# Kernel tuning notes

Measured on AMD Instinct MI355X. Metric: run time of the kernel, lower is better.

## Reference

```python
import jax, jax.numpy as jnp
import numpy as np

WD, WH, WW = 2, 7, 7          # window size (D,H,W)
NH = 3                        # num heads
DIM = 96                      # channels
N = WD * WH * WW              # tokens per window = 98
HD = DIM // NH                # head dim = 32
MLP_HID = int(DIM * 4.0)
EPS = 1e-5


def _rel_index():
    coords = np.stack(np.meshgrid(np.arange(WD), np.arange(WH), np.arange(WW), indexing='ij')).reshape(3, -1)
    rel = (coords[:, :, None] - coords[:, None, :]).transpose(1, 2, 0)  # (N,N,3)
    rel[:, :, 0] += WD - 1
    rel[:, :, 1] += WH - 1
    rel[:, :, 2] += WW - 1
    rel[:, :, 0] *= (2 * WH - 1) * (2 * WW - 1)
    rel[:, :, 1] *= 2 * WW - 1
    return rel.sum(-1)  # (N,N) int

REL_IDX = jnp.asarray(_rel_index())


def setup_inputs() -> dict:
    key = jax.random.key(0)
    ks = jax.random.split(key, 8)
    s = 0.02
    return {
        'x': jax.random.normal(ks[0], (8, 8, 56, 56, DIM), jnp.float32),
        'norm1_w': jnp.ones((DIM,), jnp.float32),
        'norm1_b': jnp.zeros((DIM,), jnp.float32),
        'qkv_w': jax.random.normal(ks[1], (3 * DIM, DIM), jnp.float32) * s,
        'qkv_b': jnp.zeros((3 * DIM,), jnp.float32),
        'proj_w': jax.random.normal(ks[2], (DIM, DIM), jnp.float32) * s,
        'proj_b': jnp.zeros((DIM,), jnp.float32),
        'rpb_table': jax.random.normal(ks[3], ((2 * WD - 1) * (2 * WH - 1) * (2 * WW - 1), NH), jnp.float32) * s,
        'norm2_w': jnp.ones((DIM,), jnp.float32),
        'norm2_b': jnp.zeros((DIM,), jnp.float32),
        'fc1_w': jax.random.normal(ks[4], (MLP_HID, DIM), jnp.float32) * s,
        'fc1_b': jnp.zeros((MLP_HID,), jnp.float32),
        'fc2_w': jax.random.normal(ks[5], (DIM, MLP_HID), jnp.float32) * s,
        'fc2_b': jnp.zeros((DIM,), jnp.float32),
    }


def _layernorm(x, w, b):
    m = x.mean(-1, keepdims=True)
    v = ((x - m) ** 2).mean(-1, keepdims=True)
    return (x - m) * jax.lax.rsqrt(v + EPS) * w + b


def _window_partition(x):
    B, D, H, W, C = x.shape
    x = x.reshape(B, D // WD, WD, H // WH, WH, W // WW, WW, C)
    return x.transpose(0, 1, 3, 5, 2, 4, 6, 7).reshape(-1, N, C)


def _window_reverse(win, B, D, H, W):
    x = win.reshape(B, D // WD, H // WH, W // WW, WD, WH, WW, -1)
    return x.transpose(0, 1, 4, 2, 5, 3, 6, 7).reshape(B, D, H, W, -1)


def reference(x, norm1_w, norm1_b, qkv_w, qkv_b, proj_w, proj_b, rpb_table,
              norm2_w, norm2_b, fc1_w, fc1_b, fc2_w, fc2_b):
    B, D, H, W, C = x.shape
    shortcut = x
    xn = _layernorm(x, norm1_w, norm1_b)
    xw = _window_partition(xn)                       # (Bw, N, C)
    Bw = xw.shape[0]

    qkv = xw @ qkv_w.T + qkv_b                       # (Bw, N, 3C)
    qkv = qkv.reshape(Bw, N, 3, NH, HD).transpose(2, 0, 3, 1, 4)
    q, k, v = qkv[0], qkv[1], qkv[2]                 # (Bw, NH, N, HD)
    scale = HD ** -0.5
    attn = jnp.einsum('bhnd,bhmd->bhnm', q * scale, k)
    bias = rpb_table[REL_IDX].transpose(2, 0, 1)     # (NH, N, N)
    attn = jax.nn.softmax(attn + bias[None], axis=-1)
    out = jnp.einsum('bhnm,bhmd->bhnd', attn, v)
    out = out.transpose(0, 2, 1, 3).reshape(Bw, N, C)
    out = out @ proj_w.T + proj_b

    x = shortcut + _window_reverse(out, B, D, H, W)
    h = _layernorm(x, norm2_w, norm2_b)
    h = jax.nn.gelu(h @ fc1_w.T + fc1_b, approximate=False)
    x = x + (h @ fc2_w.T + fc2_b)
    return x
```

## Files before the change

### kernel.cpp

```cpp
#include <hip/hip_runtime.h>
#include <hip/hip_bf16.h>
#include <math.h>


#define NTOK 98
#define SCALE 0.17677669529663687f

#define FR_PROJ 54
#define FR_FC1  72
#define FR_FC2  144
#define WS_BF16_N 110592
#define WS_BIASM_BYTE 221184
#define WS_NEED   296448

typedef __attribute__((ext_vector_type(8))) short bf16x8;
typedef __attribute__((ext_vector_type(4))) float f32x4;

__device__ __forceinline__ int row_of(int wid, int t) {
    int b = wid >> 8, rem = wid & 255;
    int d0 = rem >> 6, h0 = (rem >> 3) & 7, w0 = rem & 7;
    int td = t / 49, tr = t % 49, th = tr / 7, tw = tr % 7;
    int dd = d0 * 2 + td, hh = h0 * 7 + th, ww = w0 * 7 + tw;
    return ((b * 8 + dd) * 56 + hh) * 56 + ww;
}

__device__ __forceinline__ int pcode(int t) {
    int a = t / 49, r = t - 49 * a, b = r / 7, c = r - 7 * b;
    return a * 169 + b * 13 + c;
}

__device__ __forceinline__ unsigned short f2bfu(float f) {
    __hip_bfloat16 h = __float2bfloat16(f);
    unsigned short u; __builtin_memcpy(&u, &h, 2); return u;
}
__device__ __forceinline__ unsigned int pk2(float lo, float hi) {
    return (unsigned int)f2bfu(lo) | ((unsigned int)f2bfu(hi) << 16);
}
__device__ __forceinline__ float bl16(unsigned int u) {
    union { unsigned int i; float f; } c; c.i = u << 16; return c.f;
}
__device__ __forceinline__ float bh16(unsigned int u) {
    union { unsigned int i; float f; } c; c.i = u & 0xffff0000u; return c.f;
}
__device__ __forceinline__ bf16x8 loadB_sw(const __hip_bfloat16* wsb, int frag, int lane) {
    return *(const bf16x8*)(wsb + (frag << 9) + (lane << 3));
}
__device__ __forceinline__ bf16x8 ldsFrag(const __hip_bfloat16* base, int frag, int lane) {
    return *(const bf16x8*)(base + (frag << 9) + (lane << 3));
}
__device__ __forceinline__ bf16x8 loadB_f32(const float* wf, int idx) {
    bf16x8 r;
    #pragma unroll
    for (int j = 0; j < 8; ++j) r[j] = (short)f2bfu(wf[idx + j]);
    return r;
}
__device__ __forceinline__ float gelu(float v) {
    return 0.5f * v * (1.f + erff(v * 0.70710678118654752f));
}

__global__ __launch_bounds__(256) void prep_kernel(
    const float* __restrict__ qkv_w, const float* __restrict__ proj_w,
    const float* __restrict__ fc1_w, const float* __restrict__ fc2_w,
    const float* __restrict__ rpb,
    __hip_bfloat16* __restrict__ wsb, __hip_bfloat16* __restrict__ biasMb)
{
    int i = blockIdx.x * 256 + threadIdx.x;
    if (i < WS_BF16_N) {
        int f = i >> 9, lane = (i >> 3) & 63, j = i & 7;
        int l15 = lane & 15, g = lane >> 4;
        float v;
        if (f < FR_PROJ) {
            int ks = f % 3, nt = (f / 3) % 6, c = f / 18;
            v = qkv_w[(c * 96 + nt * 16 + l15) * 96 + ks * 32 + g * 8 + j];
            if (c == 0) v *= SCALE;
        } else if (f < FR_FC1) {
            int f2 = f - FR_PROJ, ks = f2 % 3, nt = f2 / 3;
            v = proj_w[(nt * 16 + l15) * 96 + ks * 32 + g * 8 + j];
        } else if (f < FR_FC2) {
            int f2 = f - FR_FC1, ks = f2 % 3, nt = (f2 / 3) % 4, hc = f2 / 12;
            v = fc1_w[(hc * 64 + nt * 16 + l15) * 96 + ks * 32 + g * 8 + j];
        } else {
            int f2 = f - FR_FC2, p = f2 & 1, nt = (f2 >> 1) % 6, hc = f2 / 12;
            v = fc2_w[(nt * 16 + l15) * 384 + hc * 64 + p * 32 + g * 8 + j];
        }
        wsb[i] = __float2bfloat16(v);
    } else if (i < WS_BF16_N + 37632) {
        int j = i - WS_BF16_N;
        int r = j & 3, lane = (j >> 2) & 63;
        int rest = j >> 8;
        int U = rest % 7; rest /= 7;
        int Tt = rest % 7, h = rest / 7;
        int t = Tt * 16 + (lane & 15);              if (t > 97) t = 97;
        int u = U * 16 + ((lane >> 4) << 2) + r;    if (u > 97) u = 97;
        biasMb[j] = __float2bfloat16(rpb[(pcode(t) - pcode(u) + 253) * 3 + h]);
    }
}

__global__ __launch_bounds__(512, 4) void fused_kernel(
    const float* __restrict__ x,
    const float* __restrict__ n1w, const float* __restrict__ n1b,
    const float* __restrict__ qkv_w, const float* __restrict__ qkv_b,
    const float* __restrict__ proj_w, const float* __restrict__ proj_b,
    const float* __restrict__ rpb,
    const float* __restrict__ n2w, const float* __restrict__ n2b,
    const float* __restrict__ w1, const float* __restrict__ b1,
    const float* __restrict__ w2, const float* __restrict__ b2,
    const __hip_bfloat16* __restrict__ wsb, const __hip_bfloat16* __restrict__ biasMb,
    int usews,
    float* __restrict__ out)
{
    __shared__ __align__(16) unsigned char LB[72704];
    __shared__ int rowbase[NTOK];
    __hip_bfloat16 (*XS)[104] = (__hip_bfloat16 (*)[104])LB;
    __hip_bfloat16 (*Kb)[104] = (__hip_bfloat16 (*)[104])(LB + 23296);
    __hip_bfloat16* VQ = (__hip_bfloat16*)(LB + 46592);
    __hip_bfloat16* S0 = (__hip_bfloat16*)(LB + 23296);
    __hip_bfloat16* S1 = (__hip_bfloat16*)(LB + 47872);

    const int wid = blockIdx.x, tid = threadIdx.x;
    const int lane = tid & 63, wv = tid >> 6;
    const int l15 = lane & 15;
    const int g = lane >> 4;
    const int koff = g * 8;
    const int drow = g * 4;
    const bool oddg = (g >> 1) & 1;
    const int srcA = l15 + ((g & 1) << 5);
    const int srcB = srcA + 16;

    for (int t = tid; t < NTOK; t += 512) rowbase[t] = row_of(wid, t) * 96;
    for (int i = tid; i < 14 * 104; i += 512) {
        int r = 98 + i / 104, c = i % 104;
        XS[r][c] = __float2bfloat16(0.f);
    }
    if (usews) {
        const int4* s = (const int4*)wsb;
        int4* d = (int4*)S0;
        for (int i = tid; i < 1152; i += 512) d[i] = s[i];
    }

    {
        float w0 = n1w[lane], b0 = n1b[lane];
        float w1_ = (lane < 32) ? n1w[64 + lane] : 0.f;
        float b1_ = (lane < 32) ? n1b[64 + lane] : 0.f;
        for (int t = wv; t < NTOK; t += 8) {
            int base = row_of(wid, t) * 96;
            float v0 = x[base + lane];
            float v1 = (lane < 32) ? x[base + 64 + lane] : 0.f;
            float s = v0 + v1;
            #pragma unroll
            for (int m = 32; m; m >>= 1) s += __shfl_xor(s, m, 64);
            float mean = s * (1.f / 96.f);
            float e0 = v0 - mean;
            float e1 = (lane < 32) ? (v1 - mean) : 0.f;
            float ss = e0 * e0 + e1 * e1;
            #pragma unroll
            for (int m = 32; m; m >>= 1) ss += __shfl_xor(ss, m, 64);
            float rstd = rsqrtf(ss * (1.f / 96.f) + 1e-5f);
            XS[t][lane] = __float2bfloat16(e0 * rstd * w0 + b0);
            if (lane < 32)
                XS[t][64 + lane] = __float2bfloat16(e1 * rstd * w1_ + b1_);
        }
    }
    __syncthreads();

    __hip_bfloat16* QB = &VQ[0];
    for (int tile = wv; tile < 42; tile += 8) {
        int m0 = (tile / 6) * 16, nt = tile % 6, n0 = nt * 16;
        f32x4 acc = {0.f, 0.f, 0.f, 0.f};
        #pragma unroll
        for (int ks = 0; ks < 3; ++ks) {
            bf16x8 a = *(const bf16x8*)&XS[m0 + l15][ks * 32 + koff];
            bf16x8 b = usews ? ldsFrag(S0, nt * 3 + ks, lane)
                             : loadB_f32(qkv_w, (n0 + l15) * 96 + ks * 32 + koff);
            acc = __builtin_amdgcn_mfma_f32_16x16x32_bf16(a, b, acc, 0, 0, 0);
        }
        float bb = qkv_b[n0 + l15];
        #pragma unroll
        for (int r = 0; r < 4; ++r) {
            float q = usews ? (acc[r] + bb * SCALE) : ((acc[r] + bb) * SCALE);
            QB[(m0 + drow + r) * 104 + n0 + l15] = __float2bfloat16(q);
        }
    }
    __syncthreads();

    bf16x8 qf[3];
    #pragma unroll
    for (int i = 0; i < 3; ++i) {
        int task = wv + 8 * i;
        if (task < 21) {
            int s_ = task / 3, h_ = task - 3 * s_;
            qf[i] = *(const bf16x8*)&QB[(s_ * 16 + l15) * 104 + h_ * 32 + koff];
        }
    }
    __syncthreads();

    __hip_bfloat16* vT = &VQ[0];
    for (int i = tid; i < 96 * 38; i += 512) {
        int r = i / 38, c = 98 + (i - r * 38);
        vT[r * 136 + c] = __float2bfloat16(0.f);
    }
    for (int c = 1; c < 3; ++c) {
        for (int tile = wv; tile < 42; tile += 8) {
            int m0 = (tile / 6) * 16, nt = tile % 6, n0 = nt * 16;
            f32x4 acc = {0.f, 0.f, 0.f, 0.f};
            #pragma unroll
            for (int ks = 0; ks < 3; ++ks) {
                bf16x8 a = *(const bf16x8*)&XS[m0 + l15][ks * 32 + koff];
                bf16x8 b = usews ? loadB_sw(wsb, (c * 6 + nt) * 3 + ks, lane)
                                 : loadB_f32(qkv_w + c * 9216,
                                             (n0 + l15) * 96 + ks * 32 + koff);
                acc = __builtin_amdgcn_mfma_f32_16x16x32_bf16(a, b, acc, 0, 0, 0);
            }
            float bb = qkv_b[c * 96 + n0 + l15];
            if (c == 1) {
                #pragma unroll
                for (int r = 0; r < 4; ++r)
                    Kb[m0 + drow + r][n0 + l15] = __float2bfloat16(acc[r] + bb);
            } else {
                unsigned int d0 = pk2(acc[0] + bb, acc[1] + bb);
                unsigned int d1 = pk2(acc[2] + bb, acc[3] + bb);
                int u0 = m0 + drow;
                if (u0 < NTOK) {
                    unsigned int* p = (unsigned int*)&vT[(n0 + l15) * 136 + u0];
                    p[0] = d0;
                    if (u0 + 2 < NTOK) p[1] = d1;
                }
            }
        }
    }
    __syncthreads();

    #pragma unroll 1
    for (int i = 0; i < 3; ++i) {
        int task = wv + 8 * i;
        if (task >= 21) break;
        int strip = task / 3, h = task - 3 * strip;

        f32x4 s[7];
        #pragma unroll
        for (int U = 0; U < 7; ++U) {
            bf16x8 ak = *(const bf16x8*)&Kb[U * 16 + l15][h * 32 + koff];
            f32x4 z = {0.f, 0.f, 0.f, 0.f};
            s[U] = __builtin_amdgcn_mfma_f32_16x16x32_bf16(ak, qf[i], z, 0, 0, 0);
        }
        if (usews) {
            const __hip_bfloat16* bmb = biasMb + (((h * 7 + strip) * 7) << 8) + (lane << 2);
            #pragma unroll
            for (int U = 0; U < 7; ++U) {
                uint2 bv = *(const uint2*)(bmb + (U << 8));
                s[U][0] += bl16(bv.x); s[U][1] += bh16(bv.x);
                s[U][2] += bl16(bv.y); s[U][3] += bh16(bv.y);
            }
        } else {
            int tq = strip * 16 + l15; if (tq > 97) tq = 97;
            int pt = pcode(tq);
            #pragma unroll
            for (int U = 0; U < 7; ++U)
                #pragma unroll
                for (int r = 0; r < 4; ++r) {
                    int u = U * 16 + drow + r; if (u > 97) u = 97;
                    s[U][r] += rpb[(pt - pcode(u) + 253) * 3 + h];
                }
        }
        if (drow > 0) { s[6][0] = -1e30f; s[6][1] = -1e30f; }
        s[6][2] = -1e30f; s[6][3] = -1e30f;
        f32x4 sumv = {0.f, 0.f, 0.f, 0.f};
        #pragma unroll
        for (int U = 0; U < 7; ++U) {
            #pragma unroll
            for (int r = 0; r < 4; ++r) { s[U][r] = __expf(s[U][r]); sumv[r] += s[U][r]; }
        }
        float hs = sumv[0] + sumv[1] + sumv[2] + sumv[3];
        hs += __shfl_xor(hs, 16, 64);
        hs += __shfl_xor(hs, 32, 64);
        float inv = 1.f / hs;
        unsigned int dwl[7], dwh[7];
        #pragma unroll
        for (int U = 0; U < 7; ++U) {
            dwl[U] = pk2(s[U][0] * inv, s[U][1] * inv);
            dwh[U] = pk2(s[U][2] * inv, s[U][3] * inv);
        }
        f32x4 acc0 = {0.f, 0.f, 0.f, 0.f}, acc1 = {0.f, 0.f, 0.f, 0.f};
        #pragma unroll
        for (int ks = 0; ks < 4; ++ks) {
            unsigned int D0, D1, D2, D3;
            if (ks < 3) {
                unsigned int e0 = __shfl((int)dwl[2 * ks], srcA, 64);
                unsigned int o0 = __shfl((int)dwl[2 * ks + 1], srcA, 64);
                unsigned int e1 = __shfl((int)dwh[2 * ks], srcA, 64);
                unsigned int o1 = __shfl((int)dwh[2 * ks + 1], srcA, 64);
                unsigned int e2 = __shfl((int)dwl[2 * ks], srcB, 64);
                unsigned int o2 = __shfl((int)dwl[2 * ks + 1], srcB, 64);
                unsigned int e3 = __shfl((int)dwh[2 * ks], srcB, 64);
                unsigned int o3 = __shfl((int)dwh[2 * ks + 1], srcB, 64);
                D0 = oddg ? o0 : e0; D1 = oddg ? o1 : e1;
                D2 = oddg ? o2 : e2; D3 = oddg ? o3 : e3;
            } else {
                unsigned int t0 = __shfl((int)dwl[6], srcA, 64);
                unsigned int t1 = __shfl((int)dwh[6], srcA, 64);
                unsigned int t2 = __shfl((int)dwl[6], srcB, 64);
                unsigned int t3 = __shfl((int)dwh[6], srcB, 64);
                D0 = (g < 2) ? t0 : 0u; D1 = (g < 2) ? t1 : 0u;
                D2 = (g < 2) ? t2 : 0u; D3 = (g < 2) ? t3 : 0u;
            }
            union { unsigned int d[4]; bf16x8 v; } af;
            af.d[0] = D0; af.d[1] = D1; af.d[2] = D2; af.d[3] = D3;
            bf16x8 b0 = *(const bf16x8*)&vT[(h * 32 + l15) * 136 + ks * 32 + koff];
            bf16x8 b1_ = *(const bf16x8*)&vT[(h * 32 + 16 + l15) * 136 + ks * 32 + koff];
            acc0 = __builtin_amdgcn_mfma_f32_16x16x32_bf16(af.v, b0, acc0, 0, 0, 0);
            acc1 = __builtin_amdgcn_mfma_f32_16x16x32_bf16(af.v, b1_, acc1, 0, 0, 0);
        }
        #pragma unroll
        for (int r = 0; r < 4; ++r) {
            XS[strip * 16 + drow + r][h * 32 + l15]      = __float2bfloat16(acc0[r]);
            XS[strip * 16 + drow + r][h * 32 + 16 + l15] = __float2bfloat16(acc1[r]);
        }
    }
    __syncthreads();

    if (usews) {
        const int4* sp = (const int4*)(wsb + (FR_PROJ << 9));
        int4* d0 = (int4*)S0;
        for (int i = tid; i < 1152; i += 512) d0[i] = sp[i];
        const int4* s1 = (const int4*)(wsb + (FR_FC1 << 9));
        const int4* s2 = (const int4*)(wsb + (FR_FC2 << 9));
        int4* d1 = (int4*)S1;
        for (int i = tid; i < 768; i += 512) d1[i] = s1[i];
        for (int i = tid; i < 768; i += 512) d1[768 + i] = s2[i];
    }
    __syncthreads();

    float res[6][4];
    f32x4 yacc[6];
    const int m0 = wv * 16;
    if (wv < 7) {
        f32x4 sAcc = {0.f, 0.f, 0.f, 0.f}, sqAcc = {0.f, 0.f, 0.f, 0.f};
        #pragma unroll
        for (int nt = 0; nt < 6; ++nt) {
            f32x4 acc = {0.f, 0.f, 0.f, 0.f};
            #pragma unroll
            for (int ks = 0; ks < 3; ++ks) {
                bf16x8 a = *(const bf16x8*)&XS[m0 + l15][ks * 32 + koff];
                bf16x8 b = usews ? ldsFrag(S0, nt * 3 + ks, lane)
                                 : loadB_f32(proj_w, (nt * 16 + l15) * 96 + ks * 32 + koff);
                acc = __builtin_amdgcn_mfma_f32_16x16x32_bf16(a, b, acc, 0, 0, 0);
            }
            float pb = proj_b[nt * 16 + l15];
            #pragma unroll
            for (int r = 0; r < 4; ++r) {
                int t = m0 + drow + r;
                float rv = (t < NTOK) ? (acc[r] + pb + x[rowbase[t] + nt * 16 + l15]) : 0.f;
                res[nt][r] = rv;
                sAcc[r] += rv; sqAcc[r] += rv * rv;
            }
        }
        #pragma unroll
        for (int r = 0; r < 4; ++r) {
            float s = sAcc[r], sq = sqAcc[r];
            #pragma unroll
            for (int m = 1; m < 16; m <<= 1) {
                s  += __shfl_xor(s, m, 64);
                sq += __shfl_xor(sq, m, 64);
            }
            float mean = s * (1.f / 96.f);
            float var = sq * (1.f / 96.f) - mean * mean;
            float rstd = rsqrtf(var + 1e-5f);
            #pragma unroll
            for (int nt = 0; nt < 6; ++nt) {
                int cc = nt * 16 + l15;
                XS[m0 + drow + r][cc] =
                    __float2bfloat16((res[nt][r] - mean) * rstd * n2w[cc] + n2b[cc]);
            }
        }
        #pragma unroll
        for (int nt = 0; nt < 6; ++nt) yacc[nt] = (f32x4){0.f, 0.f, 0.f, 0.f};
    }

    #pragma unroll 1
    for (int hc = 0; hc < 6; ++hc) {
        __syncthreads();
        if (wv == 7) {
            if (usews && hc < 5) {
                int4* d = (int4*)((hc & 1) ? S1 : S0);
                const int4* s1 = (const int4*)(wsb + ((FR_FC1 + (hc + 1) * 12) << 9));
                const int4* s2 = (const int4*)(wsb + ((FR_FC2 + (hc + 1) * 12) << 9));
                for (int i = lane; i < 768; i += 64) d[i] = s1[i];
                for (int i = lane; i < 768; i += 64) d[768 + i] = s2[i];
            }
        } else {
            const __hip_bfloat16* WB = (hc & 1) ? S0 : S1;
            #pragma unroll
            for (int p = 0; p < 2; ++p) {
                f32x4 s0 = {0.f, 0.f, 0.f, 0.f}, s1v = {0.f, 0.f, 0.f, 0.f};
                #pragma unroll
                for (int ks = 0; ks < 3; ++ks) {
                    bf16x8 xb = *(const bf16x8*)&XS[m0 + l15][ks * 32 + koff];
                    bf16x8 aw0 = usews ? ldsFrag(WB, (2 * p) * 3 + ks, lane)
                                       : loadB_f32(w1, (hc * 64 + 2 * p * 16 + l15) * 96 + ks * 32 + koff);
                    bf16x8 aw1 = usews ? ldsFrag(WB, (2 * p + 1) * 3 + ks, lane)
                                       : loadB_f32(w1, (hc * 64 + (2 * p + 1) * 16 + l15) * 96 + ks * 32 + koff);
                    s0  = __builtin_amdgcn_mfma_f32_16x16x32_bf16(aw0, xb, s0, 0, 0, 0);
                    s1v = __builtin_amdgcn_mfma_f32_16x16x32_bf16(aw1, xb, s1v, 0, 0, 0);
                }
                f32x4 bv0 = *(const f32x4*)&b1[hc * 64 + 2 * p * 16 + drow];
                f32x4 bv1 = *(const f32x4*)&b1[hc * 64 + (2 * p + 1) * 16 + drow];
                unsigned int dl0 = pk2(gelu(s0[0] + bv0[0]), gelu(s0[1] + bv0[1]));
                unsigned int dh0 = pk2(gelu(s0[2] + bv0[2]), gelu(s0[3] + bv0[3]));
                unsigned int dl1 = pk2(gelu(s1v[0] + bv1[0]), gelu(s1v[1] + bv1[1]));
                unsigned int dh1 = pk2(gelu(s1v[2] + bv1[2]), gelu(s1v[3] + bv1[3]));

                unsigned int e0 = __shfl((int)dl0, srcA, 64);
                unsigned int o0 = __shfl((int)dl1, srcA, 64);
                unsigned int e1 = __shfl((int)dh0, srcA, 64);
                unsigned int o1 = __shfl((int)dh1, srcA, 64);
                unsigned int e2 = __shfl((int)dl0, srcB, 64);
                unsigned int o2 = __shfl((int)dl1, srcB, 64);
                unsigned int e3 = __shfl((int)dh0, srcB, 64);
                unsigned int o3 = __shfl((int)dh1, srcB, 64);
                union { unsigned int d[4]; bf16x8 v; } af;
                af.d[0] = oddg ? o0 : e0;
                af.d[1] = oddg ? o1 : e1;
                af.d[2] = oddg ? o2 : e2;
                af.d[3] = oddg ? o3 : e3;
                #pragma unroll
                for (int nt = 0; nt < 6; ++nt) {
                    bf16x8 bw = usews ? ldsFrag(WB, 12 + nt * 2 + p, lane)
                                      : loadB_f32(w2, (nt * 16 + l15) * 384 + hc * 64 + p * 32 + koff);
                    yacc[nt] = __builtin_amdgcn_mfma_f32_16x16x32_bf16(af.v, bw, yacc[nt], 0, 0, 0);
                }
            }
        }
    }

    if (wv < 7) {
        #pragma unroll
        for (int nt = 0; nt < 6; ++nt) {
            float bb2 = b2[nt * 16 + l15];
            #pragma unroll
            for (int r = 0; r < 4; ++r) {
                int t = m0 + drow + r;
                if (t < NTOK)
                    out[rowbase[t] + nt * 16 + l15] = res[nt][r] + yacc[nt][r] + bb2;
            }
        }
    }
}

extern "C" void kernel_launch(void* const* d_in, const int* in_sizes, int n_in,
                              void* d_out, int out_size, void* d_ws, size_t ws_size,
                              hipStream_t stream) {
    const float* x      = (const float*)d_in[0];
    const float* n1w    = (const float*)d_in[1];
    const float* n1b    = (const float*)d_in[2];
    const float* qkv_w  = (const float*)d_in[3];
    const float* qkv_b  = (const float*)d_in[4];
    const float* proj_w = (const float*)d_in[5];
    const float* proj_b = (const float*)d_in[6];
    const float* rpb    = (const float*)d_in[7];
    const float* n2w    = (const float*)d_in[8];
    const float* n2b    = (const float*)d_in[9];
    const float* fc1_w  = (const float*)d_in[10];
    const float* fc1_b  = (const float*)d_in[11];
    const float* fc2_w  = (const float*)d_in[12];
    const float* fc2_b  = (const float*)d_in[13];
    float* out = (float*)d_out;

    const int usews = (ws_size >= (size_t)WS_NEED) ? 1 : 0;
    __hip_bfloat16* wsb = (__hip_bfloat16*)d_ws;
    __hip_bfloat16* biasMb = (__hip_bfloat16*)((char*)d_ws + WS_BIASM_BYTE);

    if (usews)
        prep_kernel<<<(WS_BF16_N + 37632 + 255) / 256, 256, 0, stream>>>(
            qkv_w, proj_w, fc1_w, fc2_w, rpb, wsb, biasMb);

    fused_kernel<<<2048, 512, 0, stream>>>(x, n1w, n1b, qkv_w, qkv_b,
                                           proj_w, proj_b, rpb,
                                           n2w, n2b, fc1_w, fc1_b, fc2_w, fc2_b,
                                           wsb, biasMb, usews, out);
}
```

Baseline: 335.7 us.

## Give each wave a fixed row strip, drop LDS weight staging, shrink LDS

The kernel now runs 7 waves per block, each owning one 16-token strip end to end: QKV, all three heads of attention, projection, LN2 and the MLP. The LDS copies of weight fragments and the producer-wave double buffering for fc1/fc2 are removed, so B fragments are read directly from the global workspace and rely on L1/L2 caching. This cuts LDS from about 72KB to about 49KB so more blocks fit per CU, and it removes several barriers. In exchange, per-wave global weight traffic goes up, and the residual is now stored as bf16 in LDS instead of being kept in fp32 registers, which loses accuracy in the residual path.

```diff
diff --git a/kernel.cpp b/kernel.cpp
--- a/kernel.cpp
+++ b/kernel.cpp
@@ -44,9 +44,6 @@
 }
 __device__ __forceinline__ bf16x8 loadB_sw(const __hip_bfloat16* wsb, int frag, int lane) {
     return *(const bf16x8*)(wsb + (frag << 9) + (lane << 3));
-}
-__device__ __forceinline__ bf16x8 ldsFrag(const __hip_bfloat16* base, int frag, int lane) {
-    return *(const bf16x8*)(base + (frag << 9) + (lane << 3));
 }
 __device__ __forceinline__ bf16x8 loadB_f32(const float* wf, int idx) {
     bf16x8 r;
@@ -96,7 +93,7 @@
     }
 }
 
-__global__ __launch_bounds__(512, 4) void fused_kernel(
+__global__ __launch_bounds__(448, 6) void fused_kernel(
     const float* __restrict__ x,
     const float* __restrict__ n1w, const float* __restrict__ n1b,
     const float* __restrict__ qkv_w, const float* __restrict__ qkv_b,
@@ -109,13 +106,10 @@
     int usews,
     float* __restrict__ out)
 {
-    __shared__ __align__(16) unsigned char LB[72704];
+    __shared__ __align__(16) unsigned char LB[49408];
     __shared__ int rowbase[NTOK];
     __hip_bfloat16 (*XS)[104] = (__hip_bfloat16 (*)[104])LB;
-    __hip_bfloat16 (*Kb)[104] = (__hip_bfloat16 (*)[104])(LB + 23296);
-    __hip_bfloat16* VQ = (__hip_bfloat16*)(LB + 46592);
-    __hip_bfloat16* S0 = (__hip_bfloat16*)(LB + 23296);
-    __hip_bfloat16* S1 = (__hip_bfloat16*)(LB + 47872);
+    __hip_bfloat16* RB = (__hip_bfloat16*)(LB + 23296);
 
     const int wid = blockIdx.x, tid = threadIdx.x;
     const int lane = tid & 63, wv = tid >> 6;
@@ -126,23 +120,19 @@
     const bool oddg = (g >> 1) & 1;
     const int srcA = l15 + ((g & 1) << 5);
     const int srcB = srcA + 16;
-
-    for (int t = tid; t < NTOK; t += 512) rowbase[t] = row_of(wid, t) * 96;
-    for (int i = tid; i < 14 * 104; i += 512) {
+    const int m0 = wv * 16;
+
+    for (int t = tid; t < NTOK; t += 448) rowbase[t] = row_of(wid, t) * 96;
+    for (int i = tid; i < 14 * 104; i += 448) {
         int r = 98 + i / 104, c = i % 104;
         XS[r][c] = __float2bfloat16(0.f);
-    }
-    if (usews) {
-        const int4* s = (const int4*)wsb;
-        int4* d = (int4*)S0;
-        for (int i = tid; i < 1152; i += 512) d[i] = s[i];
     }
 
     {
         float w0 = n1w[lane], b0 = n1b[lane];
         float w1_ = (lane < 32) ? n1w[64 + lane] : 0.f;
         float b1_ = (lane < 32) ? n1b[64 + lane] : 0.f;
-        for (int t = wv; t < NTOK; t += 8) {
+        for (int t = wv; t < NTOK; t += 7) {
             int base = row_of(wid, t) * 96;
             float v0 = x[base + lane];
             float v1 = (lane < 32) ? x[base + 64 + lane] : 0.f;
@@ -163,88 +153,94 @@
     }
     __syncthreads();
 
-    __hip_bfloat16* QB = &VQ[0];
-    for (int tile = wv; tile < 42; tile += 8) {
-        int m0 = (tile / 6) * 16, nt = tile % 6, n0 = nt * 16;
+    bf16x8 ax0 = *(const bf16x8*)&XS[m0 + l15][koff];
+    bf16x8 ax1 = *(const bf16x8*)&XS[m0 + l15][32 + koff];
+    bf16x8 ax2 = *(const bf16x8*)&XS[m0 + l15][64 + koff];
+
+    __hip_bfloat16* QB = RB;
+    #pragma unroll
+    for (int nt = 0; nt < 6; ++nt) {
         f32x4 acc = {0.f, 0.f, 0.f, 0.f};
-        #pragma unroll
-        for (int ks = 0; ks < 3; ++ks) {
-            bf16x8 a = *(const bf16x8*)&XS[m0 + l15][ks * 32 + koff];
-            bf16x8 b = usews ? ldsFrag(S0, nt * 3 + ks, lane)
-                             : loadB_f32(qkv_w, (n0 + l15) * 96 + ks * 32 + koff);
-            acc = __builtin_amdgcn_mfma_f32_16x16x32_bf16(a, b, acc, 0, 0, 0);
-        }
-        float bb = qkv_b[n0 + l15];
+        acc = __builtin_amdgcn_mfma_f32_16x16x32_bf16(ax0,
+              usews ? loadB_sw(wsb, nt * 3 + 0, lane)
+                    : loadB_f32(qkv_w, (nt * 16 + l15) * 96 + koff), acc, 0, 0, 0);
+        acc = __builtin_amdgcn_mfma_f32_16x16x32_bf16(ax1,
+              usews ? loadB_sw(wsb, nt * 3 + 1, lane)
+                    : loadB_f32(qkv_w, (nt * 16 + l15) * 96 + 32 + koff), acc, 0, 0, 0);
+        acc = __builtin_amdgcn_mfma_f32_16x16x32_bf16(ax2,
+              usews ? loadB_sw(wsb, nt * 3 + 2, lane)
+                    : loadB_f32(qkv_w, (nt * 16 + l15) * 96 + 64 + koff), acc, 0, 0, 0);
+        float bb = qkv_b[nt * 16 + l15];
         #pragma unroll
         for (int r = 0; r < 4; ++r) {
             float q = usews ? (acc[r] + bb * SCALE) : ((acc[r] + bb) * SCALE);
-            QB[(m0 + drow + r) * 104 + n0 + l15] = __float2bfloat16(q);
-        }
-    }
+            QB[(m0 + drow + r) * 104 + nt * 16 + l15] = __float2bfloat16(q);
+        }
+    }
+    bf16x8 qf0 = *(const bf16x8*)&QB[(m0 + l15) * 104 + koff];
+    bf16x8 qf1 = *(const bf16x8*)&QB[(m0 + l15) * 104 + 32 + koff];
+    bf16x8 qf2 = *(const bf16x8*)&QB[(m0 + l15) * 104 + 64 + koff];
     __syncthreads();
 
-    bf16x8 qf[3];
-    #pragma unroll
-    for (int i = 0; i < 3; ++i) {
-        int task = wv + 8 * i;
-        if (task < 21) {
-            int s_ = task / 3, h_ = task - 3 * s_;
-            qf[i] = *(const bf16x8*)&QB[(s_ * 16 + l15) * 104 + h_ * 32 + koff];
-        }
-    }
-    __syncthreads();
-
-    __hip_bfloat16* vT = &VQ[0];
-    for (int i = tid; i < 96 * 38; i += 512) {
+    __hip_bfloat16* vT = RB;
+    for (int i = tid; i < 96 * 38; i += 448) {
         int r = i / 38, c = 98 + (i - r * 38);
         vT[r * 136 + c] = __float2bfloat16(0.f);
     }
-    for (int c = 1; c < 3; ++c) {
-        for (int tile = wv; tile < 42; tile += 8) {
-            int m0 = (tile / 6) * 16, nt = tile % 6, n0 = nt * 16;
-            f32x4 acc = {0.f, 0.f, 0.f, 0.f};
-            #pragma unroll
-            for (int ks = 0; ks < 3; ++ks) {
-                bf16x8 a = *(const bf16x8*)&XS[m0 + l15][ks * 32 + koff];
-                bf16x8 b = usews ? loadB_sw(wsb, (c * 6 + nt) * 3 + ks, lane)
-                                 : loadB_f32(qkv_w + c * 9216,
-                                             (n0 + l15) * 96 + ks * 32 + koff);
-                acc = __builtin_amdgcn_mfma_f32_16x16x32_bf16(a, b, acc, 0, 0, 0);
-            }
-            float bb = qkv_b[c * 96 + n0 + l15];
-            if (c == 1) {
-                #pragma unroll
-                for (int r = 0; r < 4; ++r)
-                    Kb[m0 + drow + r][n0 + l15] = __float2bfloat16(acc[r] + bb);
-            } else {
-                unsigned int d0 = pk2(acc[0] + bb, acc[1] + bb);
-                unsigned int d1 = pk2(acc[2] + bb, acc[3] + bb);
-                int u0 = m0 + drow;
-                if (u0 < NTOK) {
-                    unsigned int* p = (unsigned int*)&vT[(n0 + l15) * 136 + u0];
-                    p[0] = d0;
-                    if (u0 + 2 < NTOK) p[1] = d1;
-                }
-            }
-        }
+    #pragma unroll
+    for (int nt = 0; nt < 6; ++nt) {
+        f32x4 acc = {0.f, 0.f, 0.f, 0.f};
+        acc = __builtin_amdgcn_mfma_f32_16x16x32_bf16(ax0,
+              usews ? loadB_sw(wsb, (12 + nt) * 3 + 0, lane)
+                    : loadB_f32(qkv_w + 18432, (nt * 16 + l15) * 96 + koff), acc, 0, 0, 0);
+        acc = __builtin_amdgcn_mfma_f32_16x16x32_bf16(ax1,
+              usews ? loadB_sw(wsb, (12 + nt) * 3 + 1, lane)
+                    : loadB_f32(qkv_w + 18432, (nt * 16 + l15) * 96 + 32 + koff), acc, 0, 0, 0);
+        acc = __builtin_amdgcn_mfma_f32_16x16x32_bf16(ax2,
+              usews ? loadB_sw(wsb, (12 + nt) * 3 + 2, lane)
+                    : loadB_f32(qkv_w + 18432, (nt * 16 + l15) * 96 + 64 + koff), acc, 0, 0, 0);
+        float bb = qkv_b[192 + nt * 16 + l15];
+        unsigned int d0 = pk2(acc[0] + bb, acc[1] + bb);
+        unsigned int d1 = pk2(acc[2] + bb, acc[3] + bb);
+        int u0 = m0 + drow;
+        if (u0 < NTOK) {
+            unsigned int* p = (unsigned int*)&vT[(nt * 16 + l15) * 136 + u0];
+            p[0] = d0;
+            if (u0 + 2 < NTOK) p[1] = d1;
+        }
+    }
+    #pragma unroll
+    for (int nt = 0; nt < 6; ++nt) {
+        f32x4 acc = {0.f, 0.f, 0.f, 0.f};
+        acc = __builtin_amdgcn_mfma_f32_16x16x32_bf16(ax0,
+              usews ? loadB_sw(wsb, (6 + nt) * 3 + 0, lane)
+                    : loadB_f32(qkv_w + 9216, (nt * 16 + l15) * 96 + koff), acc, 0, 0, 0);
+        acc = __builtin_amdgcn_mfma_f32_16x16x32_bf16(ax1,
+              usews ? loadB_sw(wsb, (6 + nt) * 3 + 1, lane)
+                    : loadB_f32(qkv_w + 9216, (nt * 16 + l15) * 96 + 32 + koff), acc, 0, 0, 0);
+        acc = __builtin_amdgcn_mfma_f32_16x16x32_bf16(ax2,
+              usews ? loadB_sw(wsb, (6 + nt) * 3 + 2, lane)
+                    : loadB_f32(qkv_w + 9216, (nt * 16 + l15) * 96 + 64 + koff), acc, 0, 0, 0);
+        float bb = qkv_b[96 + nt * 16 + l15];
+        #pragma unroll
+        for (int r = 0; r < 4; ++r)
+            XS[m0 + drow + r][nt * 16 + l15] = __float2bfloat16(acc[r] + bb);
     }
     __syncthreads();
 
+    unsigned int po[3][4];
     #pragma unroll 1
-    for (int i = 0; i < 3; ++i) {
-        int task = wv + 8 * i;
-        if (task >= 21) break;
-        int strip = task / 3, h = task - 3 * strip;
-
+    for (int h = 0; h < 3; ++h) {
+        bf16x8 qh = (h == 0) ? qf0 : (h == 1) ? qf1 : qf2;
         f32x4 s[7];
         #pragma unroll
         for (int U = 0; U < 7; ++U) {
-            bf16x8 ak = *(const bf16x8*)&Kb[U * 16 + l15][h * 32 + koff];
+            bf16x8 ak = *(const bf16x8*)&XS[U * 16 + l15][h * 32 + koff];
             f32x4 z = {0.f, 0.f, 0.f, 0.f};
-            s[U] = __builtin_amdgcn_mfma_f32_16x16x32_bf16(ak, qf[i], z, 0, 0, 0);
+            s[U] = __builtin_amdgcn_mfma_f32_16x16x32_bf16(ak, qh, z, 0, 0, 0);
         }
         if (usews) {
-            const __hip_bfloat16* bmb = biasMb + (((h * 7 + strip) * 7) << 8) + (lane << 2);
+            const __hip_bfloat16* bmb = biasMb + (((h * 7 + wv) * 7) << 8) + (lane << 2);
             #pragma unroll
             for (int U = 0; U < 7; ++U) {
                 uint2 bv = *(const uint2*)(bmb + (U << 8));
@@ -252,7 +248,7 @@
                 s[U][2] += bl16(bv.y); s[U][3] += bh16(bv.y);
             }
         } else {
-            int tq = strip * 16 + l15; if (tq > 97) tq = 97;
+            int tq = wv * 16 + l15; if (tq > 97) tq = 97;
             int pt = pcode(tq);
             #pragma unroll
             for (int U = 0; U < 7; ++U)
@@ -280,21 +276,21 @@
             dwl[U] = pk2(s[U][0] * inv, s[U][1] * inv);
             dwh[U] = pk2(s[U][2] * inv, s[U][3] * inv);
         }
-        f32x4 acc0 = {0.f, 0.f, 0.f, 0.f}, acc1 = {0.f, 0.f, 0.f, 0.f};
+        f32x4 o0 = {0.f, 0.f, 0.f, 0.f}, o1 = {0.f, 0.f, 0.f, 0.f};
         #pragma unroll
         for (int ks = 0; ks < 4; ++ks) {
             unsigned int D0, D1, D2, D3;
             if (ks < 3) {
                 unsigned int e0 = __shfl((int)dwl[2 * ks], srcA, 64);
-                unsigned int o0 = __shfl((int)dwl[2 * ks + 1], srcA, 64);
+                unsigned int q0 = __shfl((int)dwl[2 * ks + 1], srcA, 64);
                 unsigned int e1 = __shfl((int)dwh[2 * ks], srcA, 64);
-                unsigned int o1 = __shfl((int)dwh[2 * ks + 1], srcA, 64);
+                unsigned int q1 = __shfl((int)dwh[2 * ks + 1], srcA, 64);
                 unsigned int e2 = __shfl((int)dwl[2 * ks], srcB, 64);
-                unsigned int o2 = __shfl((int)dwl[2 * ks + 1], srcB, 64);
+                unsigned int q2 = __shfl((int)dwl[2 * ks + 1], srcB, 64);
                 unsigned int e3 = __shfl((int)dwh[2 * ks], srcB, 64);
-                unsigned int o3 = __shfl((int)dwh[2 * ks + 1], srcB, 64);
-                D0 = oddg ? o0 : e0; D1 = oddg ? o1 : e1;
-                D2 = oddg ? o2 : e2; D3 = oddg ? o3 : e3;
+                unsigned int q3 = __shfl((int)dwh[2 * ks + 1], srcB, 64);
+                D0 = oddg ? q0 : e0; D1 = oddg ? q1 : e1;
+                D2 = oddg ? q2 : e2; D3 = oddg ? q3 : e3;
             } else {
                 unsigned int t0 = __shfl((int)dwl[6], srcA, 64);
                 unsigned int t1 = __shfl((int)dwh[6], srcA, 64);
@@ -305,142 +301,140 @@
             }
             union { unsigned int d[4]; bf16x8 v; } af;
             af.d[0] = D0; af.d[1] = D1; af.d[2] = D2; af.d[3] = D3;
-            bf16x8 b0 = *(const bf16x8*)&vT[(h * 32 + l15) * 136 + ks * 32 + koff];
-            bf16x8 b1_ = *(const bf16x8*)&vT[(h * 32 + 16 + l15) * 136 + ks * 32 + koff];
-            acc0 = __builtin_amdgcn_mfma_f32_16x16x32_bf16(af.v, b0, acc0, 0, 0, 0);
-            acc1 = __builtin_amdgcn_mfma_f32_16x16x32_bf16(af.v, b1_, acc1, 0, 0, 0);
-        }
+            bf16x8 va = *(const bf16x8*)&vT[(h * 32 + l15) * 136 + ks * 32 + koff];
+            bf16x8 vb = *(const bf16x8*)&vT[(h * 32 + 16 + l15) * 136 + ks * 32 + koff];
+            o0 = __builtin_amdgcn_mfma_f32_16x16x32_bf16(va, af.v, o0, 0, 0, 0);
+            o1 = __builtin_amdgcn_mfma_f32_16x16x32_bf16(vb, af.v, o1, 0, 0, 0);
+        }
+        po[h][0] = pk2(o0[0], o0[1]); po[h][1] = pk2(o0[2], o0[3]);
+        po[h][2] = pk2(o1[0], o1[1]); po[h][3] = pk2(o1[2], o1[3]);
+    }
+
+    union { unsigned int d[4]; bf16x8 v; } afO[3];
+    #pragma unroll
+    for (int h = 0; h < 3; ++h) {
+        unsigned int e0 = __shfl((int)po[h][0], srcA, 64);
+        unsigned int q0 = __shfl((int)po[h][2], srcA, 64);
+        unsigned int e1 = __shfl((int)po[h][1], srcA, 64);
+        unsigned int q1 = __shfl((int)po[h][3], srcA, 64);
+        unsigned int e2 = __shfl((int)po[h][0], srcB, 64);
+        unsigned int q2 = __shfl((int)po[h][2], srcB, 64);
+        unsigned int e3 = __shfl((int)po[h][1], srcB, 64);
+        unsigned int q3 = __shfl((int)po[h][3], srcB, 64);
+        afO[h].d[0] = oddg ? q0 : e0;
+        afO[h].d[1] = oddg ? q1 : e1;
+        afO[h].d[2] = oddg ? q2 : e2;
+        afO[h].d[3] = oddg ? q3 : e3;
+    }
+
+    float res[6][4];
+    f32x4 sAcc = {0.f, 0.f, 0.f, 0.f}, sqAcc = {0.f, 0.f, 0.f, 0.f};
+    #pragma unroll
+    for (int nt = 0; nt < 6; ++nt) {
+        f32x4 acc = {0.f, 0.f, 0.f, 0.f};
+        #pragma unroll
+        for (int h = 0; h < 3; ++h) {
+            bf16x8 b = usews ? loadB_sw(wsb, FR_PROJ + nt * 3 + h, lane)
+                             : loadB_f32(proj_w, (nt * 16 + l15) * 96 + h * 32 + koff);
+            acc = __builtin_amdgcn_mfma_f32_16x16x32_bf16(afO[h].v, b, acc, 0, 0, 0);
+        }
+        float pb = proj_b[nt * 16 + l15];
         #pragma unroll
         for (int r = 0; r < 4; ++r) {
-            XS[strip * 16 + drow + r][h * 32 + l15]      = __float2bfloat16(acc0[r]);
-            XS[strip * 16 + drow + r][h * 32 + 16 + l15] = __float2bfloat16(acc1[r]);
-        }
+            int t = m0 + drow + r;
+            float rv = (t < NTOK) ? (acc[r] + pb + x[rowbase[t] + nt * 16 + l15]) : 0.f;
+            res[nt][r] = rv;
+            sAcc[r] += rv; sqAcc[r] += rv * rv;
+        }
+    }
+    float mean[4], rstd[4];
+    #pragma unroll
+    for (int r = 0; r < 4; ++r) {
+        float s = sAcc[r], sq = sqAcc[r];
+        #pragma unroll
+        for (int m = 1; m < 16; m <<= 1) {
+            s  += __shfl_xor(s, m, 64);
+            sq += __shfl_xor(sq, m, 64);
+        }
+        mean[r] = s * (1.f / 96.f);
+        float var = sq * (1.f / 96.f) - mean[r] * mean[r];
+        rstd[r] = rsqrtf(var + 1e-5f);
     }
     __syncthreads();
 
-    if (usews) {
-        const int4* sp = (const int4*)(wsb + (FR_PROJ << 9));
-        int4* d0 = (int4*)S0;
-        for (int i = tid; i < 1152; i += 512) d0[i] = sp[i];
-        const int4* s1 = (const int4*)(wsb + (FR_FC1 << 9));
-        const int4* s2 = (const int4*)(wsb + (FR_FC2 << 9));
-        int4* d1 = (int4*)S1;
-        for (int i = tid; i < 768; i += 512) d1[i] = s1[i];
-        for (int i = tid; i < 768; i += 512) d1[768 + i] = s2[i];
-    }
-    __syncthreads();
-
-    float res[6][4];
+    __hip_bfloat16* resB = RB;
+    #pragma unroll
+    for (int nt = 0; nt < 6; ++nt) {
+        int cc = nt * 16 + l15;
+        float w2_ = n2w[cc], b2_ = n2b[cc];
+        #pragma unroll
+        for (int r = 0; r < 4; ++r) {
+            XS[m0 + drow + r][cc] =
+                __float2bfloat16((res[nt][r] - mean[r]) * rstd[r] * w2_ + b2_);
+            resB[(m0 + drow + r) * 104 + cc] = __float2bfloat16(res[nt][r]);
+        }
+    }
+
+    bf16x8 xb0 = *(const bf16x8*)&XS[m0 + l15][koff];
+    bf16x8 xb1 = *(const bf16x8*)&XS[m0 + l15][32 + koff];
+    bf16x8 xb2 = *(const bf16x8*)&XS[m0 + l15][64 + koff];
     f32x4 yacc[6];
-    const int m0 = wv * 16;
-    if (wv < 7) {
-        f32x4 sAcc = {0.f, 0.f, 0.f, 0.f}, sqAcc = {0.f, 0.f, 0.f, 0.f};
-        #pragma unroll
-        for (int nt = 0; nt < 6; ++nt) {
-            f32x4 acc = {0.f, 0.f, 0.f, 0.f};
-            #pragma unroll
-            for (int ks = 0; ks < 3; ++ks) {
-                bf16x8 a = *(const bf16x8*)&XS[m0 + l15][ks * 32 + koff];
-                bf16x8 b = usews ? ldsFrag(S0, nt * 3 + ks, lane)
-                                 : loadB_f32(proj_w, (nt * 16 + l15) * 96 + ks * 32 + koff);
-                acc = __builtin_amdgcn_mfma_f32_16x16x32_bf16(a, b, acc, 0, 0, 0);
-            }
-            float pb = proj_b[nt * 16 + l15];
-            #pragma unroll
-            for (int r = 0; r < 4; ++r) {
-                int t = m0 + drow + r;
-                float rv = (t < NTOK) ? (acc[r] + pb + x[rowbase[t] + nt * 16 + l15]) : 0.f;
-                res[nt][r] = rv;
-                sAcc[r] += rv; sqAcc[r] += rv * rv;
-            }
-        }
-        #pragma unroll
-        for (int r = 0; r < 4; ++r) {
-            float s = sAcc[r], sq = sqAcc[r];
-            #pragma unroll
-            for (int m = 1; m < 16; m <<= 1) {
-                s  += __shfl_xor(s, m, 64);
-                sq += __shfl_xor(sq, m, 64);
-            }
-            float mean = s * (1.f / 96.f);
-            float var = sq * (1.f / 96.f) - mean * mean;
-            float rstd = rsqrtf(var + 1e-5f);
-            #pragma unroll
-            for (int nt = 0; nt < 6; ++nt) {
-                int cc = nt * 16 + l15;
-                XS[m0 + drow + r][cc] =
-                    __float2bfloat16((res[nt][r] - mean) * rstd * n2w[cc] + n2b[cc]);
-            }
-        }
-        #pragma unroll
-        for (int nt = 0; nt < 6; ++nt) yacc[nt] = (f32x4){0.f, 0.f, 0.f, 0.f};
-    }
+    #pragma unroll
+    for (int nt = 0; nt < 6; ++nt) yacc[nt] = (f32x4){0.f, 0.f, 0.f, 0.f};
 
     #pragma unroll 1
     for (int hc = 0; hc < 6; ++hc) {
-        __syncthreads();
-        if (wv == 7) {
-            if (usews && hc < 5) {
-                int4* d = (int4*)((hc & 1) ? S1 : S0);
-                const int4* s1 = (const int4*)(wsb + ((FR_FC1 + (hc + 1) * 12) << 9));
-                const int4* s2 = (const int4*)(wsb + ((FR_FC2 + (hc + 1) * 12) << 9));
-                for (int i = lane; i < 768; i += 64) d[i] = s1[i];
-                for (int i = lane; i < 768; i += 64) d[768 + i] = s2[i];
+        #pragma unroll
+        for (int p = 0; p < 2; ++p) {
+            f32x4 s0 = {0.f, 0.f, 0.f, 0.f}, s1v = {0.f, 0.f, 0.f, 0.f};
+            #pragma unroll
+            for (int ks = 0; ks < 3; ++ks) {
+                bf16x8 xb = (ks == 0) ? xb0 : (ks == 1) ? xb1 : xb2;
+                bf16x8 aw0 = usews ? loadB_sw(wsb, FR_FC1 + (hc * 4 + 2 * p) * 3 + ks, lane)
+                                   : loadB_f32(w1, (hc * 64 + 2 * p * 16 + l15) * 96 + ks * 32 + koff);
+                bf16x8 aw1 = usews ? loadB_sw(wsb, FR_FC1 + (hc * 4 + 2 * p + 1) * 3 + ks, lane)
+                                   : loadB_f32(w1, (hc * 64 + (2 * p + 1) * 16 + l15) * 96 + ks * 32 + koff);
+                s0  = __builtin_amdgcn_mfma_f32_16x16x32_bf16(aw0, xb, s0, 0, 0, 0);
+                s1v = __builtin_amdgcn_mfma_f32_16x16x32_bf16(aw1, xb, s1v, 0, 0, 0);
             }
-        } else {
-            const __hip_bfloat16* WB = (hc & 1) ? S0 : S1;
-            #pragma unroll
-            for (int p = 0; p < 2; ++p) {
-                f32x4 s0 = {0.f, 0.f, 0.f, 0.f}, s1v = {0.f, 0.f, 0.f, 0.f};
-                #pragma unroll
-                for (int ks = 0; ks < 3; ++ks) {
-                    bf16x8 xb = *(const bf16x8*)&XS[m0 + l15][ks * 32 + koff];
-                    bf16x8 aw0 = usews ? ldsFrag(WB, (2 * p) * 3 + ks, lane)
-                                       : loadB_f32(w1, (hc * 64 + 2 * p * 16 + l15) * 96 + ks * 32 + koff);
-                    bf16x8 aw1 = usews ? ldsFrag(WB, (2 * p + 1) * 3 + ks, lane)
-                                       : loadB_f32(w1, (hc * 64 + (2 * p + 1) * 16 + l15) * 96 + ks * 32 + koff);
-                    s0  = __builtin_amdgcn_mfma_f32_16x16x32_bf16(aw0, xb, s0, 0, 0, 0);
-                    s1v = __builtin_amdgcn_mfma_f32_16x16x32_bf16(aw1, xb, s1v, 0, 0, 0);
-                }
-                f32x4 bv0 = *(const f32x4*)&b1[hc * 64 + 2 * p * 16 + drow];
-                f32x4 bv1 = *(const f32x4*)&b1[hc * 64 + (2 * p + 1) * 16 + drow];
-                unsigned int dl0 = pk2(gelu(s0[0] + bv0[0]), gelu(s0[1] + bv0[1]));
-                unsigned int dh0 = pk2(gelu(s0[2] + bv0[2]), gelu(s0[3] + bv0[3]));
-                unsigned int dl1 = pk2(gelu(s1v[0] + bv1[0]), gelu(s1v[1] + bv1[1]));
-                unsigned int dh1 = pk2(gelu(s1v[2] + bv1[2]), gelu(s1v[3] + bv1[3]));
-
-                unsigned int e0 = __shfl((int)dl0, srcA, 64);
-                unsigned int o0 = __shfl((int)dl1, srcA, 64);
-                unsigned int e1 = __shfl((int)dh0, srcA, 64);
-                unsigned int o1 = __shfl((int)dh1, srcA, 64);
-                unsigned int e2 = __shfl((int)dl0, srcB, 64);
-                unsigned int o2 = __shfl((int)dl1, srcB, 64);
-                unsigned int e3 = __shfl((int)dh0, srcB, 64);
-                unsigned int o3 = __shfl((int)dh1, srcB, 64);
-                union { unsigned int d[4]; bf16x8 v; } af;
-                af.d[0] = oddg ? o0 : e0;
-                af.d[1] = oddg ? o1 : e1;
-                af.d[2] = oddg ? o2 : e2;
-                af.d[3] = oddg ? o3 : e3;
-                #pragma unroll
-                for (int nt = 0; nt < 6; ++nt) {
-                    bf16x8 bw = usews ? ldsFrag(WB, 12 + nt * 2 + p, lane)
-                                      : loadB_f32(w2, (nt * 16 + l15) * 384 + hc * 64 + p * 32 + koff);
-                    yacc[nt] = __builtin_amdgcn_mfma_f32_16x16x32_bf16(af.v, bw, yacc[nt], 0, 0, 0);
-                }
+            f32x4 bv0 = *(const f32x4*)&b1[hc * 64 + 2 * p * 16 + drow];
+            f32x4 bv1 = *(const f32x4*)&b1[hc * 64 + (2 * p + 1) * 16 + drow];
+            unsigned int dl0 = pk2(gelu(s0[0] + bv0[0]), gelu(s0[1] + bv0[1]));
+            unsigned int dh0 = pk2(gelu(s0[2] + bv0[2]), gelu(s0[3] + bv0[3]));
+            unsigned int dl1 = pk2(gelu(s1v[0] + bv1[0]), gelu(s1v[1] + bv1[1]));
+            unsigned int dh1 = pk2(gelu(s1v[2] + bv1[2]), gelu(s1v[3] + bv1[3]));
+
+            unsigned int e0 = __shfl((int)dl0, srcA, 64);
+            unsigned int q0 = __shfl((int)dl1, srcA, 64);
+            unsigned int e1 = __shfl((int)dh0, srcA, 64);
+            unsigned int q1 = __shfl((int)dh1, srcA, 64);
+            unsigned int e2 = __shfl((int)dl0, srcB, 64);
+            unsigned int q2 = __shfl((int)dl1, srcB, 64);
+            unsigned int e3 = __shfl((int)dh0, srcB, 64);
+            unsigned int q3 = __shfl((int)dh1, srcB, 64);
+            union { unsigned int d[4]; bf16x8 v; } af;
+            af.d[0] = oddg ? q0 : e0;
+            af.d[1] = oddg ? q1 : e1;
+            af.d[2] = oddg ? q2 : e2;
+            af.d[3] = oddg ? q3 : e3;
+            #pragma unroll
+            for (int nt = 0; nt < 6; ++nt) {
+                bf16x8 bw = usews ? loadB_sw(wsb, FR_FC2 + hc * 12 + nt * 2 + p, lane)
+                                  : loadB_f32(w2, (nt * 16 + l15) * 384 + hc * 64 + p * 32 + koff);
+                yacc[nt] = __builtin_amdgcn_mfma_f32_16x16x32_bf16(af.v, bw, yacc[nt], 0, 0, 0);
             }
         }
     }
 
-    if (wv < 7) {
-        #pragma unroll
-        for (int nt = 0; nt < 6; ++nt) {
-            float bb2 = b2[nt * 16 + l15];
-            #pragma unroll
-            for (int r = 0; r < 4; ++r) {
-                int t = m0 + drow + r;
-                if (t < NTOK)
-                    out[rowbase[t] + nt * 16 + l15] = res[nt][r] + yacc[nt][r] + bb2;
+    #pragma unroll
+    for (int nt = 0; nt < 6; ++nt) {
+        float bb2 = b2[nt * 16 + l15];
+        #pragma unroll
+        for (int r = 0; r < 4; ++r) {
+            int t = m0 + drow + r;
+            if (t < NTOK) {
+                float rv = __bfloat162float(resB[t * 104 + nt * 16 + l15]);
+                out[rowbase[t] + nt * 16 + l15] = rv + yacc[nt][r] + bb2;
             }
         }
     }
@@ -473,7 +467,7 @@
         prep_kernel<<<(WS_BF16_N + 37632 + 255) / 256, 256, 0, stream>>>(
             qkv_w, proj_w, fc1_w, fc2_w, rpb, wsb, biasMb);
 
-    fused_kernel<<<2048, 512, 0, stream>>>(x, n1w, n1b, qkv_w, qkv_b,
+    fused_kernel<<<2048, 448, 0, stream>>>(x, n1w, n1b, qkv_w, qkv_b,
                                            proj_w, proj_b, rpb,
                                            n2w, n2b, fc1_w, fc1_b, fc2_w, fc2_b,
                                            wsb, biasMb, usews, out);
```

New measurement: 412.8 us. 1.23x slower.
